# Kernel optimization log

Measured on AMD Instinct MI355X. Metric: run time of the kernel, lower is better.

The kernel has to match this reference:

```python
import jax, jax.numpy as jnp
import numpy as np

B, T, N, D = 64, 10, 64, 4      # batch, time steps, num_vars, input_size
H = 128                          # encoder_hidden
K = 2                            # num_edge_types
EPS = 1e-5                       # BatchNorm eps
_edges = np.ones((N, N)) - np.eye(N)
SEND = jnp.asarray(np.where(_edges)[0])   # [E], E = N*(N-1)
RECV = jnp.asarray(np.where(_edges)[1])   # [E]


def _xavier(key, shape):
    std = (2.0 / (shape[0] + shape[1])) ** 0.5
    return std * jax.random.normal(key, shape, dtype=jnp.float32)


def _mlp(x, w1, b1, w2, b2, g, beta):
    # RefNRIMLP: Linear -> ELU -> (dropout p=0) -> Linear -> ELU -> BatchNorm1d
    h = jax.nn.elu(x @ w1 + b1)
    h = jax.nn.elu(h @ w2 + b2)
    flat = h.reshape(-1, h.shape[-1])  # BN over flattened (batch*objects) axis
    mu = flat.mean(0)
    var = flat.var(0)
    flat = (flat - mu) * jax.lax.rsqrt(var + EPS) * g + beta
    return flat.reshape(h.shape)


def setup_inputs() -> dict:
    key = jax.random.key(0)
    ks = jax.random.split(key, 10)
    inp = {"inputs": jax.random.normal(ks[0], (B, T, N, D), dtype=jnp.float32)}
    fan_ins = {"mlp1": T * D, "mlp2": 2 * H, "mlp3": H, "mlp4": 3 * H}
    for i, (name, nin) in enumerate(fan_ins.items()):
        k1, k2 = jax.random.split(ks[i + 1])
        inp[name + "_w1"] = _xavier(k1, (nin, H))
        inp[name + "_b1"] = jnp.full((H,), 0.1, dtype=jnp.float32)
        inp[name + "_w2"] = _xavier(k2, (H, H))
        inp[name + "_b2"] = jnp.full((H,), 0.1, dtype=jnp.float32)
        inp[name + "_g"] = jnp.ones((H,), dtype=jnp.float32)
        inp[name + "_beta"] = jnp.zeros((H,), dtype=jnp.float32)
    inp["fc_w"] = _xavier(ks[9], (H, K))
    inp["fc_b"] = jnp.full((K,), 0.1, dtype=jnp.float32)
    return inp


def reference(inputs, mlp1_w1, mlp1_b1, mlp1_w2, mlp1_b2, mlp1_g, mlp1_beta,
              mlp2_w1, mlp2_b1, mlp2_w2, mlp2_b2, mlp2_g, mlp2_beta,
              mlp3_w1, mlp3_b1, mlp3_w2, mlp3_b2, mlp3_g, mlp3_beta,
              mlp4_w1, mlp4_b1, mlp4_w2, mlp4_b2, mlp4_g, mlp4_beta,
              fc_w, fc_b):
    # [B,T,N,D] -> [B,N,T*D]
    x = jnp.transpose(inputs, (0, 2, 1, 3)).reshape(B, N, T * D)
    x = _mlp(x, mlp1_w1, mlp1_b1, mlp1_w2, mlp1_b2, mlp1_g, mlp1_beta)
    # node2edge: gather send/recv node embeddings, concat -> [B,E,2H]
    x = jnp.concatenate([x[:, SEND], x[:, RECV]], axis=-1)
    x = _mlp(x, mlp2_w1, mlp2_b1, mlp2_w2, mlp2_b2, mlp2_g, mlp2_beta)
    x_skip = x
    # edge2node: one-hot(recv).T matmul == segment_sum over recv index, then /(N-1)
    agg = jax.ops.segment_sum(jnp.swapaxes(x, 0, 1), RECV, num_segments=N)  # [N,B,H]
    x = jnp.swapaxes(agg, 0, 1) / (N - 1)  # [B,N,H]
    x = _mlp(x, mlp3_w1, mlp3_b1, mlp3_w2, mlp3_b2, mlp3_g, mlp3_beta)
    x = jnp.concatenate([x[:, SEND], x[:, RECV]], axis=-1)  # [B,E,2H]
    x = jnp.concatenate([x, x_skip], axis=-1)  # [B,E,3H]
    x = _mlp(x, mlp4_w1, mlp4_b1, mlp4_w2, mlp4_b2, mlp4_g, mlp4_beta)
    return x @ fc_w + fc_b  # logits [B, E, K]
```

## Files before the change

### kernel.cpp

```cpp
#include <hip/hip_runtime.h>

#define BN_EPS 1e-5f

using h8 = __attribute__((ext_vector_type(8))) _Float16;
using f4v = __attribute__((ext_vector_type(4))) float;

#define OFF_COEF 0
#define OFF_CVEC 1024
#define OFF_H1 4096
#define OFF_P2 528384
#define OFF_Q2 1052672
#define OFF_H3 1576960
#define OFF_P4 2101248
#define OFF_Q4 2625536
#define OFF_W2P 3149824
#define OFF_W4P 3158016
#define OFF_WCP 3166208
#define OFF_H4B 3174400
#define WS_BYTES 78757888ull

__device__ __forceinline__ float elu_f(float x) {
    return x > 0.f ? x : __expf(x) - 1.f;
}

__device__ __forceinline__ unsigned short bf16r(float x) {
    unsigned u = __float_as_uint(x);
    return (unsigned short)((u + 0x7fffu + ((u >> 16) & 1u)) >> 16);
}


__device__ __forceinline__ void gemm_acc(float acc[4][8], float a0, float a1, float a2,
                                         float a3, const float4 wa, const float4 wb) {
    const float w[8] = {wa.x, wa.y, wa.z, wa.w, wb.x, wb.y, wb.z, wb.w};
    const float a[4] = {a0, a1, a2, a3};
#pragma unroll
    for (int j = 0; j < 4; ++j)
#pragma unroll
        for (int u = 0; u < 8; ++u)
            acc[j][u] = fmaf(a[j], w[u], acc[j][u]);
}

__device__ __forceinline__ void gemm_globalW(const float* As, int lda,
                                             const float* __restrict__ Wg, int K,
                                             float acc[4][8], int tx, int ty) {
    const float4* Wg4 = (const float4*)Wg;
#pragma unroll 4
    for (int k = 0; k < K; ++k) {
        float a0 = As[ty * lda + k];
        float a1 = As[(ty + 16) * lda + k];
        float a2 = As[(ty + 32) * lda + k];
        float a3 = As[(ty + 48) * lda + k];
        float4 wa = Wg4[k * 32 + tx];
        float4 wb = Wg4[k * 32 + 16 + tx];
        gemm_acc(acc, a0, a1, a2, a3, wa, wb);
    }
}

__device__ __forceinline__ void bias_elu(const float acc[4][8], const float* __restrict__ bias,
                                         float vals[4][8], int tx) {
    int ca = 4 * tx, cb = 64 + 4 * tx;
    float bv[8] = {bias[ca], bias[ca + 1], bias[ca + 2], bias[ca + 3],
                   bias[cb], bias[cb + 1], bias[cb + 2], bias[cb + 3]};
#pragma unroll
    for (int j = 0; j < 4; ++j)
#pragma unroll
        for (int u = 0; u < 8; ++u)
            vals[j][u] = elu_f(acc[j][u] + bv[u]);
}

__device__ __forceinline__ void store_tile(float* __restrict__ out, int row0,
                                           const float vals[4][8], int tx, int ty) {
#pragma unroll
    for (int j = 0; j < 4; ++j) {
        int r = row0 + ty + 16 * j;
        *(float4*)(out + r * 128 + 4 * tx) =
            make_float4(vals[j][0], vals[j][1], vals[j][2], vals[j][3]);
        *(float4*)(out + r * 128 + 64 + 4 * tx) =
            make_float4(vals[j][4], vals[j][5], vals[j][6], vals[j][7]);
    }
}

__device__ __forceinline__ void stats_tail(const float vals[4][8], float* red,
                                           float* __restrict__ st, int tid, int tx, int ty) {
    float ls[8], lq[8];
#pragma unroll
    for (int u = 0; u < 8; ++u) {
        ls[u] = vals[0][u] + vals[1][u] + vals[2][u] + vals[3][u];
        lq[u] = vals[0][u] * vals[0][u] + vals[1][u] * vals[1][u] +
                vals[2][u] * vals[2][u] + vals[3][u] * vals[3][u];
    }
    __syncthreads();
    int ca = 4 * tx, cb = 64 + 4 * tx;
#pragma unroll
    for (int u = 0; u < 4; ++u) {
        red[ty * 128 + ca + u] = ls[u];
        red[2048 + ty * 128 + ca + u] = lq[u];
        red[ty * 128 + cb + u] = ls[u + 4];
        red[2048 + ty * 128 + cb + u] = lq[u + 4];
    }
    __syncthreads();
    if (tid < 128) {
        float s = 0.f, q = 0.f;
#pragma unroll
        for (int t = 0; t < 16; ++t) {
            s += red[t * 128 + tid];
            q += red[2048 + t * 128 + tid];
        }
        atomicAdd(st + tid, s);
        atomicAdd(st + 128 + tid, q);
    }
}


__device__ __forceinline__ void gemm2_gw(const _Float16* A0, const _Float16* A1,
                                         const _Float16* __restrict__ wp,
                                         f4v acc0[4][2], f4v acc1[4][2], int lane, int w) {
#pragma unroll
    for (int kc = 0; kc < 4; ++kc) {
        h8 bf0 = *(const h8*)&wp[(((w * 2 + 0) * 4 + kc) * 64 + lane) * 8];
        h8 bf1 = *(const h8*)&wp[(((w * 2 + 1) * 4 + kc) * 64 + lane) * 8];
        h8 af0[4], af1[4];
#pragma unroll
        for (int rt = 0; rt < 4; ++rt) {
            af0[rt] = *(const h8*)&A0[((rt * 4 + kc) * 64 + lane) * 8];
            af1[rt] = *(const h8*)&A1[((rt * 4 + kc) * 64 + lane) * 8];
        }
#pragma unroll
        for (int rt = 0; rt < 4; ++rt) {
            acc0[rt][0] = __builtin_amdgcn_mfma_f32_16x16x32_f16(af0[rt], bf0, acc0[rt][0], 0, 0, 0);
            acc1[rt][0] = __builtin_amdgcn_mfma_f32_16x16x32_f16(af1[rt], bf0, acc1[rt][0], 0, 0, 0);
        }
#pragma unroll
        for (int rt = 0; rt < 4; ++rt) {
            acc0[rt][1] = __builtin_amdgcn_mfma_f32_16x16x32_f16(af0[rt], bf1, acc0[rt][1], 0, 0, 0);
            acc1[rt][1] = __builtin_amdgcn_mfma_f32_16x16x32_f16(af1[rt], bf1, acc1[rt][1], 0, 0, 0);
        }
    }
}

__device__ __forceinline__ void mfma_gemm_gw(const _Float16* Afr,
                                             const _Float16* __restrict__ wp,
                                             f4v acc[4][2], int lane, int w) {
#pragma unroll
    for (int kc = 0; kc < 4; ++kc) {
        h8 bf0 = *(const h8*)&wp[(((w * 2 + 0) * 4 + kc) * 64 + lane) * 8];
        h8 bf1 = *(const h8*)&wp[(((w * 2 + 1) * 4 + kc) * 64 + lane) * 8];
        h8 af[4];
#pragma unroll
        for (int rt = 0; rt < 4; ++rt)
            af[rt] = *(const h8*)&Afr[((rt * 4 + kc) * 64 + lane) * 8];
#pragma unroll
        for (int rt = 0; rt < 4; ++rt)
            acc[rt][0] = __builtin_amdgcn_mfma_f32_16x16x32_f16(af[rt], bf0, acc[rt][0], 0, 0, 0);
#pragma unroll
        for (int rt = 0; rt < 4; ++rt)
            acc[rt][1] = __builtin_amdgcn_mfma_f32_16x16x32_f16(af[rt], bf1, acc[rt][1], 0, 0, 0);
    }
}

__device__ __forceinline__ void vals_to_afrag(_Float16* Afr, const float vals[4][2][4],
                                              int lane, int w) {
    int cl = lane & 15, quad = lane >> 4;
#pragma unroll
    for (int ctl = 0; ctl < 2; ++ctl) {
        int col = (w * 2 + ctl) * 16 + cl;
        int kc = col >> 5, o = (col >> 3) & 3, j = col & 7;
#pragma unroll
        for (int rt = 0; rt < 4; ++rt)
#pragma unroll
            for (int i = 0; i < 4; ++i) {
                int m = quad * 4 + i;
                Afr[((rt * 4 + kc) * 64 + o * 16 + m) * 8 + j] = (_Float16)vals[rt][ctl][i];
            }
    }
}


__global__ void k_prep(float* W, const float* __restrict__ w2src,
                       const float* __restrict__ w4src) {
    int blk = blockIdx.x, tid = threadIdx.x;
    if (blk < 193) {
        int i = blk * 256 + tid;
        if (i < 16384) W[OFF_P2 + i] = 0.f;
        else if (i < 32768) W[OFF_P4 + i - 16384] = 0.f;
        else if (i < 49152) W[OFF_Q4 + i - 32768] = 0.f;
        else if (i < 49280) W[OFF_CVEC + i - 49152] = 0.f;
    } else {
        int second = blk >= 201;
        const float* src = second ? w4src : w2src;
        _Float16* wp = (_Float16*)(W + (second ? OFF_W4P : OFF_W2P));
        int flat = (blk - (second ? 201 : 193)) * 256 + tid;
        int g = flat >> 6, L = flat & 63;
        int ct = g >> 2, kc = g & 3;
        int nn = ct * 16 + (L & 15), k0 = kc * 32 + (L >> 4) * 8;
        h8 v;
#pragma unroll
        for (int j = 0; j < 8; ++j) v[j] = (_Float16)src[(k0 + j) * 128 + nn];
        *(h8*)&wp[flat * 8] = v;
    }
}

__global__ void k_finalize(const float* __restrict__ sums, float* __restrict__ coef,
                           float invM, const float* __restrict__ g,
                           const float* __restrict__ beta, float* __restrict__ zbuf) {
    int c = threadIdx.x;
    float s = 0.f, q = 0.f;
#pragma unroll 8
    for (int t = 0; t < 64; ++t) {
        s += sums[t * 256 + c];
        q += sums[t * 256 + 128 + c];
    }
    float mean = s * invM;
    float var = q * invM - mean * mean;
    float a = g[c] * rsqrtf(var + BN_EPS);
    coef[c] = a;
    coef[128 + c] = beta[c] - mean * a;
    if (zbuf)
        for (int i = c; i < 16384; i += 128) zbuf[i] = 0.f;
}

__global__ __launch_bounds__(256) void k_mlp1(const float* __restrict__ x,
                                              const float* __restrict__ w1,
                                              const float* __restrict__ b1,
                                              const float* __restrict__ w2,
                                              const float* __restrict__ b2,
                                              float* __restrict__ h1, float* __restrict__ st) {
    __shared__ float Xs[64 * 44];
    __shared__ float As[64 * 132];
    int tid = threadIdx.x, tx = tid & 15, ty = tid >> 4;
    int r0 = blockIdx.x * 64;
    for (int idx = tid; idx < 64 * 40; idx += 256) {
        int r = idx / 40, k = idx - r * 40;
        int rr = r0 + r, b = rr >> 6, n = rr & 63, t = k >> 2, d = k & 3;
        Xs[r * 44 + k] = x[((b * 10 + t) * 64 + n) * 4 + d];
    }
    __syncthreads();
    float acc[4][8] = {};
    gemm_globalW(Xs, 44, w1, 40, acc, tx, ty);
    float vals[4][8];
    bias_elu(acc, b1, vals, tx);
    int ca = 4 * tx, cb = 64 + 4 * tx;
#pragma unroll
    for (int j = 0; j < 4; ++j) {
        int r = ty + 16 * j;
#pragma unroll
        for (int u = 0; u < 4; ++u) {
            As[r * 132 + ca + u] = vals[j][u];
            As[r * 132 + cb + u] = vals[j][u + 4];
        }
    }
    __syncthreads();
    float acc2[4][8] = {};
    gemm_globalW(As, 132, w2, 128, acc2, tx, ty);
    float vals2[4][8];
    bias_elu(acc2, b2, vals2, tx);
    store_tile(h1, r0, vals2, tx, ty);
    stats_tail(vals2, As, st + (blockIdx.x & 63) * 256, tid, tx, ty);
}

__global__ __launch_bounds__(256) void k_pq(const float* __restrict__ h,
                                            const float* __restrict__ coef,
                                            const float* __restrict__ w,
                                            float* __restrict__ P, float* __restrict__ Q) {
    __shared__ float As[64 * 132];
    int tid = threadIdx.x, tx = tid & 15, ty = tid >> 4;
    int half = blockIdx.x >> 6;
    int r0 = (blockIdx.x & 63) * 64;
    const float* Wg = w + half * 128 * 128;
    float* out = half ? Q : P;
    const float4* h4 = (const float4*)h;
    const float4* av = (const float4*)coef;
    const float4* cv = (const float4*)(coef + 128);
#pragma unroll
    for (int i = 0; i < 8; ++i) {
        int f4 = tid + i * 256;
        int r = f4 >> 5, c4 = f4 & 31;
        float4 hv = h4[(r0 + r) * 32 + c4];
        float4 a = av[c4], c = cv[c4];
        float4 v;
        v.x = a.x * hv.x + c.x;
        v.y = a.y * hv.y + c.y;
        v.z = a.z * hv.z + c.z;
        v.w = a.w * hv.w + c.w;
        *(float4*)(As + r * 132 + c4 * 4) = v;
    }
    __syncthreads();
    float acc[4][8] = {};
    gemm_globalW(As, 132, Wg, 128, acc, tx, ty);
#pragma unroll
    for (int j = 0; j < 4; ++j) {
        int r = r0 + ty + 16 * j;
        *(float4*)(out + r * 128 + 4 * tx) = make_float4(acc[j][0], acc[j][1], acc[j][2], acc[j][3]);
        *(float4*)(out + r * 128 + 64 + 4 * tx) = make_float4(acc[j][4], acc[j][5], acc[j][6], acc[j][7]);
    }
}

__global__ __launch_bounds__(256, 4) void k_mlp2agg(const float* __restrict__ P2,
                                                    const float* __restrict__ Q2,
                                                    const float* __restrict__ b1,
                                                    const _Float16* __restrict__ w2p,
                                                    const float* __restrict__ b2,
                                                    float* __restrict__ aggraw,
                                                    _Float16* __restrict__ h2,
                                                    float* __restrict__ st) {
    __shared__ _Float16 Afr[8192];
    int tid = threadIdx.x;
    int lane = tid & 63, w = tid >> 6;
    int b = blockIdx.x >> 6, n = blockIdx.x & 63;
    float* stc = st + (blockIdx.x & 63) * 256;
    {
        int r = lane, kc = w;
        int s = (r < 63) ? (r + (r >= n ? 1 : 0)) : n;
        const float4* Pr = (const float4*)(P2 + (b * 64 + s) * 128);
        const float4* Qr = (const float4*)(Q2 + (b * 64 + n) * 128);
        const float4* B1 = (const float4*)b1;
        int rt = r >> 4, m = r & 15;
#pragma unroll
        for (int o = 0; o < 4; ++o) {
            int c4 = kc * 8 + o * 2;
            float4 p0 = Pr[c4], q0 = Qr[c4], bb0 = B1[c4];
            float4 p1 = Pr[c4 + 1], q1 = Qr[c4 + 1], bb1 = B1[c4 + 1];
            h8 v;
            v[0] = (_Float16)elu_f(p0.x + q0.x + bb0.x);
            v[1] = (_Float16)elu_f(p0.y + q0.y + bb0.y);
            v[2] = (_Float16)elu_f(p0.z + q0.z + bb0.z);
            v[3] = (_Float16)elu_f(p0.w + q0.w + bb0.w);
            v[4] = (_Float16)elu_f(p1.x + q1.x + bb1.x);
            v[5] = (_Float16)elu_f(p1.y + q1.y + bb1.y);
            v[6] = (_Float16)elu_f(p1.z + q1.z + bb1.z);
            v[7] = (_Float16)elu_f(p1.w + q1.w + bb1.w);
            *(h8*)&Afr[((rt * 4 + kc) * 64 + o * 16 + m) * 8] = v;
        }
    }
    __syncthreads();
    f4v acc[4][2];
#pragma unroll
    for (int rt = 0; rt < 4; ++rt)
#pragma unroll
        for (int c = 0; c < 2; ++c) acc[rt][c] = (f4v){0.f, 0.f, 0.f, 0.f};
    mfma_gemm_gw(Afr, w2p, acc, lane, w);
    int cl = lane & 15, quad = lane >> 4;
    float vals[2][4][4];
#pragma unroll
    for (int ctl = 0; ctl < 2; ++ctl) {
        int col = (w * 2 + ctl) * 16 + cl;
        float bias = b2[col];
        float s1 = 0.f, s2 = 0.f;
#pragma unroll
        for (int rt = 0; rt < 4; ++rt)
#pragma unroll
            for (int i = 0; i < 4; ++i) {
                int row = rt * 16 + quad * 4 + i;
                float v = elu_f(acc[rt][ctl][i] + bias);
                if (row == 63) v = 0.f;
                vals[ctl][rt][i] = v;
                s1 += v;
                s2 += v * v;
            }
        s1 += __shfl_xor(s1, 16);
        s2 += __shfl_xor(s2, 16);
        s1 += __shfl_xor(s1, 32);
        s2 += __shfl_xor(s2, 32);
        if (quad == 0) {
            aggraw[(b * 64 + n) * 128 + col] = s1;
            atomicAdd(stc + col, s1);
            atomicAdd(stc + 128 + col, s2);
        }
    }
    __syncthreads();
    unsigned short* Tb = (unsigned short*)Afr;
#pragma unroll
    for (int ctl = 0; ctl < 2; ++ctl) {
        int col = (w * 2 + ctl) * 16 + cl;
#pragma unroll
        for (int rt = 0; rt < 4; ++rt)
#pragma unroll
            for (int i = 0; i < 4; ++i) {
                int row = rt * 16 + quad * 4 + i;
                _Float16 hv = (_Float16)vals[ctl][rt][i];
                Tb[row * 128 + col] = *(unsigned short*)&hv;
            }
    }
    __syncthreads();
    {
        int rr = tid >> 2, cq = tid & 3;
        if (rr < 63) {
            int s = rr + (rr >= n ? 1 : 0);
            int e = s * 63 + (s > n ? n : n - 1);
            unsigned short* dst = (unsigned short*)h2 + ((size_t)b * 4032 + e) * 128;
#pragma unroll
            for (int i = 0; i < 4; ++i) {
                int off = cq * 32 + i * 8;
                *(uint4*)(dst + off) = *(uint4*)&Tb[rr * 128 + off];
            }
        }
    }
}

__global__ void k_wcprep(const float* __restrict__ w41, const float* __restrict__ coef2,
                         _Float16* __restrict__ wcp, float* __restrict__ cvec) {
    int k = blockIdx.x, c = threadIdx.x;
    float wv = w41[(256 + k) * 128 + c];
    int g = (c >> 4) * 4 + (k >> 5);
    int L = ((k >> 3) & 3) * 16 + (c & 15);
    int j = k & 7;
    wcp[(g * 64 + L) * 8 + j] = (_Float16)(coef2[k] * wv);
    atomicAdd(&cvec[c], coef2[128 + k] * wv);
}

__global__ __launch_bounds__(256) void k_mlp3(const float* __restrict__ raw,
                                              const float* __restrict__ coef2,
                                              const float* __restrict__ w1,
                                              const float* __restrict__ b1,
                                              const float* __restrict__ w2,
                                              const float* __restrict__ b2,
                                              float* __restrict__ h3, float* __restrict__ st) {
    __shared__ float As[64 * 132];
    int tid = threadIdx.x, tx = tid & 15, ty = tid >> 4;
    int r0 = blockIdx.x * 64;
    const float4* in4 = (const float4*)raw;
    const float4* av = (const float4*)coef2;
    const float4* cv = (const float4*)(coef2 + 128);
    const float inv63 = 1.f / 63.f;
#pragma unroll
    for (int i = 0; i < 8; ++i) {
        int f4 = tid + i * 256;
        int r = f4 >> 5, c4 = f4 & 31;
        float4 hv = in4[(r0 + r) * 32 + c4];
        float4 a = av[c4], c = cv[c4];
        float4 v;
        v.x = a.x * hv.x * inv63 + c.x;
        v.y = a.y * hv.y * inv63 + c.y;
        v.z = a.z * hv.z * inv63 + c.z;
        v.w = a.w * hv.w * inv63 + c.w;
        *(float4*)(As + r * 132 + c4 * 4) = v;
    }
    __syncthreads();
    float acc[4][8] = {};
    gemm_globalW(As, 132, w1, 128, acc, tx, ty);
    float vals[4][8];
    bias_elu(acc, b1, vals, tx);
    __syncthreads();
    int ca = 4 * tx, cb = 64 + 4 * tx;
#pragma unroll
    for (int j = 0; j < 4; ++j) {
        int r = ty + 16 * j;
#pragma unroll
        for (int u = 0; u < 4; ++u) {
            As[r * 132 + ca + u] = vals[j][u];
            As[r * 132 + cb + u] = vals[j][u + 4];
        }
    }
    __syncthreads();
    float acc2[4][8] = {};
    gemm_globalW(As, 132, w2, 128, acc2, tx, ty);
    float vals2[4][8];
    bias_elu(acc2, b2, vals2, tx);
    store_tile(h3, r0, vals2, tx, ty);
    stats_tail(vals2, As, st + (blockIdx.x & 63) * 256, tid, tx, ty);
}

__global__ __launch_bounds__(256, 3) void k_mlp4r2(const _Float16* __restrict__ h2,
                                                   const float* __restrict__ P4,
                                                   const float* __restrict__ Q4,
                                                   const _Float16* __restrict__ wcp,
                                                   const float* __restrict__ cvec,
                                                   const float* __restrict__ b1,
                                                   const _Float16* __restrict__ w4p2,
                                                   const float* __restrict__ b2,
                                                   unsigned short* __restrict__ h4,
                                                   float* __restrict__ st) {
    __shared__ _Float16 Afr0[8192];
    __shared__ _Float16 Afr1[8192];
    int tid = threadIdx.x;
    int lane = tid & 63, w = tid >> 6, cl = lane & 15, quad = lane >> 4;
    unsigned t0 = 2u * blockIdx.x, t1 = t0 + 1u;
    unsigned b0 = t0 / 63, b1i = t1 / 63;
    unsigned e00 = (t0 - b0 * 63) * 64, e01 = (t1 - b1i * 63) * 64;
    int row00 = t0 * 64, row01 = t1 * 64;
    float* stc = st + (blockIdx.x & 63) * 256;
#pragma unroll
    for (int i = 0; i < 4; ++i) {
        int u = tid + i * 256;
        int r = u >> 4, cu = u & 15;
        int dst = (((r >> 4) * 4 + (cu >> 2)) * 64 + (cu & 3) * 16 + (r & 15)) * 8;
        *(h8*)&Afr0[dst] = *(const h8*)&h2[(size_t)(row00 + r) * 128 + cu * 8];
        *(h8*)&Afr1[dst] = *(const h8*)&h2[(size_t)(row01 + r) * 128 + cu * 8];
    }
    __syncthreads();
    f4v acc0[4][2], acc1[4][2];
#pragma unroll
    for (int rt = 0; rt < 4; ++rt)
#pragma unroll
        for (int c = 0; c < 2; ++c) {
            acc0[rt][c] = (f4v){0.f, 0.f, 0.f, 0.f};
            acc1[rt][c] = (f4v){0.f, 0.f, 0.f, 0.f};
        }
    gemm2_gw(Afr0, Afr1, wcp, acc0, acc1, lane, w);
    float v0[4][2][4], v1[4][2][4];
    {
        int col0 = w * 32 + cl, col1 = col0 + 16;
        float base0 = b1[col0] + cvec[col0];
        float base1 = b1[col1] + cvec[col1];
#pragma unroll
        for (int rt = 0; rt < 4; ++rt)
#pragma unroll
            for (int i = 0; i < 4; ++i) {
                int rr = rt * 16 + quad * 4 + i;
                {
                    unsigned e = e00 + rr;
                    unsigned s = e / 63;
                    unsigned jj = e - s * 63;
                    unsigned rv = jj + (jj >= s ? 1u : 0u);
                    const float* Pr = P4 + (b0 * 64 + s) * 128;
                    const float* Qr = Q4 + (b0 * 64 + rv) * 128;
                    v0[rt][0][i] = elu_f(acc0[rt][0][i] + Pr[col0] + Qr[col0] + base0);
                    v0[rt][1][i] = elu_f(acc0[rt][1][i] + Pr[col1] + Qr[col1] + base1);
                }
                {
                    unsigned e = e01 + rr;
                    unsigned s = e / 63;
                    unsigned jj = e - s * 63;
                    unsigned rv = jj + (jj >= s ? 1u : 0u);
                    const float* Pr = P4 + (b1i * 64 + s) * 128;
                    const float* Qr = Q4 + (b1i * 64 + rv) * 128;
                    v1[rt][0][i] = elu_f(acc1[rt][0][i] + Pr[col0] + Qr[col0] + base0);
                    v1[rt][1][i] = elu_f(acc1[rt][1][i] + Pr[col1] + Qr[col1] + base1);
                }
            }
    }
    __syncthreads();
    vals_to_afrag(Afr0, v0, lane, w);
    vals_to_afrag(Afr1, v1, lane, w);
    __syncthreads();
#pragma unroll
    for (int rt = 0; rt < 4; ++rt)
#pragma unroll
        for (int c = 0; c < 2; ++c) {
            acc0[rt][c] = (f4v){0.f, 0.f, 0.f, 0.f};
            acc1[rt][c] = (f4v){0.f, 0.f, 0.f, 0.f};
        }
    gemm2_gw(Afr0, Afr1, w4p2, acc0, acc1, lane, w);
#pragma unroll
    for (int ctl = 0; ctl < 2; ++ctl) {
        int col = (w * 2 + ctl) * 16 + cl;
        float bias = b2[col];
        float s1 = 0.f, s2 = 0.f;
#pragma unroll
        for (int rt = 0; rt < 4; ++rt)
#pragma unroll
            for (int i = 0; i < 4; ++i) {
                float va = elu_f(acc0[rt][ctl][i] + bias);
                float vb = elu_f(acc1[rt][ctl][i] + bias);
                v0[rt][ctl][i] = va;
                v1[rt][ctl][i] = vb;
                s1 += va + vb;
                s2 += va * va + vb * vb;
            }
        s1 += __shfl_xor(s1, 16);
        s2 += __shfl_xor(s2, 16);
        s1 += __shfl_xor(s1, 32);
        s2 += __shfl_xor(s2, 32);
        if (quad == 0) {
            atomicAdd(stc + col, s1);
            atomicAdd(stc + 128 + col, s2);
        }
    }
    __syncthreads();
    unsigned short* T0 = (unsigned short*)Afr0;
    unsigned short* T1 = (unsigned short*)Afr1;
#pragma unroll
    for (int ctl = 0; ctl < 2; ++ctl) {
        int col = (w * 2 + ctl) * 16 + cl;
#pragma unroll
        for (int rt = 0; rt < 4; ++rt)
#pragma unroll
            for (int i = 0; i < 4; ++i) {
                int rr = rt * 16 + quad * 4 + i;
                T0[rr * 128 + col] = bf16r(v0[rt][ctl][i]);
                T1[rr * 128 + col] = bf16r(v1[rt][ctl][i]);
            }
    }
    __syncthreads();
    {
        int rr = tid >> 2, cq = tid & 3;
#pragma unroll
        for (int i = 0; i < 4; ++i) {
            int off = rr * 128 + cq * 32 + i * 8;
            *(uint4*)(h4 + (size_t)row00 * 128 + off) = *(uint4*)&T0[off];
            *(uint4*)(h4 + (size_t)row01 * 128 + off) = *(uint4*)&T1[off];
        }
    }
}

__global__ __launch_bounds__(256) void k_out(const unsigned short* __restrict__ h4,
                                             const float* __restrict__ coef4,
                                             const float* __restrict__ fcw,
                                             const float* __restrict__ fcb,
                                             float* __restrict__ out) {
    int tid = threadIdx.x;
    int lane = tid & 31, rsub = tid >> 5;
    int row = blockIdx.x * 8 + rsub;
    uint2 u = ((const uint2*)(h4 + (size_t)row * 128))[lane];
    float x0 = __uint_as_float(u.x << 16);
    float x1 = __uint_as_float(u.x & 0xffff0000u);
    float x2 = __uint_as_float(u.y << 16);
    float x3 = __uint_as_float(u.y & 0xffff0000u);
    float4 a = ((const float4*)coef4)[lane];
    float4 c = ((const float4*)(coef4 + 128))[lane];
    x0 = a.x * x0 + c.x;
    x1 = a.y * x1 + c.y;
    x2 = a.z * x2 + c.z;
    x3 = a.w * x3 + c.w;
    const float4* W = (const float4*)(fcw + lane * 8);
    float4 w01 = W[0], w23 = W[1];
    float s0 = x0 * w01.x + x1 * w01.z + x2 * w23.x + x3 * w23.z;
    float s1 = x0 * w01.y + x1 * w01.w + x2 * w23.y + x3 * w23.w;
#pragma unroll
    for (int off = 16; off > 0; off >>= 1) {
        s0 += __shfl_down(s0, off, 32);
        s1 += __shfl_down(s1, off, 32);
    }
    if (lane == 0) {
        out[row * 2] = s0 + fcb[0];
        out[row * 2 + 1] = s1 + fcb[1];
    }
}


extern "C" void kernel_launch(void* const* d_in, const int* in_sizes, int n_in,
                              void* d_out, int out_size, void* d_ws, size_t ws_size,
                              hipStream_t stream) {
    const float* x = (const float*)d_in[0];
    const float* m1_w1 = (const float*)d_in[1];
    const float* m1_b1 = (const float*)d_in[2];
    const float* m1_w2 = (const float*)d_in[3];
    const float* m1_b2 = (const float*)d_in[4];
    const float* m1_g = (const float*)d_in[5];
    const float* m1_be = (const float*)d_in[6];
    const float* m2_w1 = (const float*)d_in[7];
    const float* m2_b1 = (const float*)d_in[8];
    const float* m2_w2 = (const float*)d_in[9];
    const float* m2_b2 = (const float*)d_in[10];
    const float* m2_g = (const float*)d_in[11];
    const float* m2_be = (const float*)d_in[12];
    const float* m3_w1 = (const float*)d_in[13];
    const float* m3_b1 = (const float*)d_in[14];
    const float* m3_w2 = (const float*)d_in[15];
    const float* m3_b2 = (const float*)d_in[16];
    const float* m3_g = (const float*)d_in[17];
    const float* m3_be = (const float*)d_in[18];
    const float* m4_w1 = (const float*)d_in[19];
    const float* m4_b1 = (const float*)d_in[20];
    const float* m4_w2 = (const float*)d_in[21];
    const float* m4_b2 = (const float*)d_in[22];
    const float* m4_g = (const float*)d_in[23];
    const float* m4_be = (const float*)d_in[24];
    const float* fc_w = (const float*)d_in[25];
    const float* fc_b = (const float*)d_in[26];
    float* out = (float*)d_out;

    float* W = (float*)d_ws;
    float* coef1 = W + OFF_COEF;
    float* coef2 = W + OFF_COEF + 256;
    float* coef3 = W + OFF_COEF + 512;
    float* coef4 = W + OFF_COEF + 768;
    float* cvec = W + OFF_CVEC;
    float* h1 = W + OFF_H1;
    float* aggraw = h1;
    float* sums4 = h1;
    float* P2 = W + OFF_P2;
    float* sums1 = P2;
    float* Q2 = W + OFF_Q2;
    float* h3 = W + OFF_H3;
    float* P4 = W + OFF_P4;
    float* sums2 = P4;
    float* Q4 = W + OFF_Q4;
    float* sums3 = Q4;
    _Float16* w2p2 = (_Float16*)(W + OFF_W2P);
    _Float16* w4p2 = (_Float16*)(W + OFF_W4P);
    _Float16* wcp = (_Float16*)(W + OFF_WCP);
    _Float16* h2f = (_Float16*)(W + OFF_H4B);
    unsigned short* h4b = (unsigned short*)(W + OFF_H4B);

    if (ws_size < WS_BYTES) return;

    k_prep<<<209, 256, 0, stream>>>(W, m2_w2, m4_w2);
    k_mlp1<<<64, 256, 0, stream>>>(x, m1_w1, m1_b1, m1_w2, m1_b2, h1, sums1);
    k_finalize<<<1, 128, 0, stream>>>(sums1, coef1, 1.f / 4096.f, m1_g, m1_be, nullptr);
    k_pq<<<128, 256, 0, stream>>>(h1, coef1, m2_w1, P2, Q2);
    k_mlp2agg<<<4096, 256, 0, stream>>>(P2, Q2, m2_b1, w2p2, m2_b2, aggraw, h2f, sums2);
    k_finalize<<<1, 128, 0, stream>>>(sums2, coef2, 1.f / 258048.f, m2_g, m2_be, nullptr);
    k_wcprep<<<128, 128, 0, stream>>>(m4_w1, coef2, wcp, cvec);
    k_mlp3<<<64, 256, 0, stream>>>(aggraw, coef2, m3_w1, m3_b1, m3_w2, m3_b2, h3, sums3);
    k_finalize<<<1, 128, 0, stream>>>(sums3, coef3, 1.f / 4096.f, m3_g, m3_be, sums4);
    k_pq<<<128, 256, 0, stream>>>(h3, coef3, m4_w1, P4, Q4);
    k_mlp4r2<<<2016, 256, 0, stream>>>(h2f, P4, Q4, wcp, cvec, m4_b1, w4p2, m4_b2,
                                       h4b, sums4);
    k_finalize<<<1, 128, 0, stream>>>(sums4, coef4, 1.f / 258048.f, m4_g, m4_be, nullptr);
    k_out<<<32256, 256, 0, stream>>>(h4b, coef4, fc_w, fc_b, out);
}
```

Before: 349.0 us.

## Process two receiver nodes per block, halve k_pq tiles, simplify index math

k_mlp2agg now handles two receiver nodes per block with two shared A-fragment buffers and the shared gemm2_gw helper, so each loaded W2 fragment feeds twice as many MFMAs and there are half as many blocks and atomics. Its occupancy hint drops from 4 to 3 to fit the doubled shared memory and accumulators. k_pq uses 32-row tiles and twice as many blocks to fill more CUs. In k_mlp4r2 the per-element division by 63 and repeated P4 loads are replaced by precomputed sender rows and a select. h4 is stored as fp16 instead of bf16, and k_out converts fp16 directly.

```diff
diff --git a/kernel.cpp b/kernel.cpp
--- a/kernel.cpp
+++ b/kernel.cpp
@@ -3,6 +3,7 @@
 #define BN_EPS 1e-5f
 
 using h8 = __attribute__((ext_vector_type(8))) _Float16;
+using h4v = __attribute__((ext_vector_type(4))) _Float16;
 using f4v = __attribute__((ext_vector_type(4))) float;
 
 #define OFF_COEF 0
@@ -23,11 +24,6 @@
     return x > 0.f ? x : __expf(x) - 1.f;
 }
 
-__device__ __forceinline__ unsigned short bf16r(float x) {
-    unsigned u = __float_as_uint(x);
-    return (unsigned short)((u + 0x7fffu + ((u >> 16) & 1u)) >> 16);
-}
-
 
 __device__ __forceinline__ void gemm_acc(float acc[4][8], float a0, float a1, float a2,
                                          float a3, const float4 wa, const float4 wb) {
@@ -138,26 +134,6 @@
     }
 }
 
-__device__ __forceinline__ void mfma_gemm_gw(const _Float16* Afr,
-                                             const _Float16* __restrict__ wp,
-                                             f4v acc[4][2], int lane, int w) {
-#pragma unroll
-    for (int kc = 0; kc < 4; ++kc) {
-        h8 bf0 = *(const h8*)&wp[(((w * 2 + 0) * 4 + kc) * 64 + lane) * 8];
-        h8 bf1 = *(const h8*)&wp[(((w * 2 + 1) * 4 + kc) * 64 + lane) * 8];
-        h8 af[4];
-#pragma unroll
-        for (int rt = 0; rt < 4; ++rt)
-            af[rt] = *(const h8*)&Afr[((rt * 4 + kc) * 64 + lane) * 8];
-#pragma unroll
-        for (int rt = 0; rt < 4; ++rt)
-            acc[rt][0] = __builtin_amdgcn_mfma_f32_16x16x32_f16(af[rt], bf0, acc[rt][0], 0, 0, 0);
-#pragma unroll
-        for (int rt = 0; rt < 4; ++rt)
-            acc[rt][1] = __builtin_amdgcn_mfma_f32_16x16x32_f16(af[rt], bf1, acc[rt][1], 0, 0, 0);
-    }
-}
-
 __device__ __forceinline__ void vals_to_afrag(_Float16* Afr, const float vals[4][2][4],
                                               int lane, int w) {
     int cl = lane & 15, quad = lane >> 4;
@@ -172,6 +148,28 @@
                 int m = quad * 4 + i;
                 Afr[((rt * 4 + kc) * 64 + o * 16 + m) * 8 + j] = (_Float16)vals[rt][ctl][i];
             }
+    }
+}
+
+__device__ __forceinline__ void stage_pair(_Float16* Afr, const float4* __restrict__ Pr,
+                                           const float4* __restrict__ Qr,
+                                           const float4* __restrict__ B1, int lane, int kc) {
+    int rt = lane >> 4, m = lane & 15;
+#pragma unroll
+    for (int o = 0; o < 4; ++o) {
+        int c4 = kc * 8 + o * 2;
+        float4 p0 = Pr[c4], q0 = Qr[c4], bb0 = B1[c4];
+        float4 p1 = Pr[c4 + 1], q1 = Qr[c4 + 1], bb1 = B1[c4 + 1];
+        h8 v;
+        v[0] = (_Float16)elu_f(p0.x + q0.x + bb0.x);
+        v[1] = (_Float16)elu_f(p0.y + q0.y + bb0.y);
+        v[2] = (_Float16)elu_f(p0.z + q0.z + bb0.z);
+        v[3] = (_Float16)elu_f(p0.w + q0.w + bb0.w);
+        v[4] = (_Float16)elu_f(p1.x + q1.x + bb1.x);
+        v[5] = (_Float16)elu_f(p1.y + q1.y + bb1.y);
+        v[6] = (_Float16)elu_f(p1.z + q1.z + bb1.z);
+        v[7] = (_Float16)elu_f(p1.w + q1.w + bb1.w);
+        *(h8*)&Afr[((rt * 4 + kc) * 64 + o * 16 + m) * 8] = v;
     }
 }
 
@@ -262,17 +260,17 @@
                                             const float* __restrict__ coef,
                                             const float* __restrict__ w,
                                             float* __restrict__ P, float* __restrict__ Q) {
-    __shared__ float As[64 * 132];
+    __shared__ float As[32 * 132];
     int tid = threadIdx.x, tx = tid & 15, ty = tid >> 4;
-    int half = blockIdx.x >> 6;
-    int r0 = (blockIdx.x & 63) * 64;
+    int half = blockIdx.x >> 7;
+    int r0 = (blockIdx.x & 127) * 32;
     const float* Wg = w + half * 128 * 128;
     float* out = half ? Q : P;
     const float4* h4 = (const float4*)h;
     const float4* av = (const float4*)coef;
     const float4* cv = (const float4*)(coef + 128);
 #pragma unroll
-    for (int i = 0; i < 8; ++i) {
+    for (int i = 0; i < 4; ++i) {
         int f4 = tid + i * 256;
         int r = f4 >> 5, c4 = f4 & 31;
         float4 hv = h4[(r0 + r) * 32 + c4];
@@ -285,17 +283,30 @@
         *(float4*)(As + r * 132 + c4 * 4) = v;
     }
     __syncthreads();
-    float acc[4][8] = {};
-    gemm_globalW(As, 132, Wg, 128, acc, tx, ty);
-#pragma unroll
-    for (int j = 0; j < 4; ++j) {
+    float acc[2][8] = {};
+    const float4* Wg4 = (const float4*)Wg;
+#pragma unroll 4
+    for (int k = 0; k < 128; ++k) {
+        float a0 = As[ty * 132 + k];
+        float a1 = As[(ty + 16) * 132 + k];
+        float4 wa = Wg4[k * 32 + tx];
+        float4 wb = Wg4[k * 32 + 16 + tx];
+        const float wv[8] = {wa.x, wa.y, wa.z, wa.w, wb.x, wb.y, wb.z, wb.w};
+#pragma unroll
+        for (int u = 0; u < 8; ++u) {
+            acc[0][u] = fmaf(a0, wv[u], acc[0][u]);
+            acc[1][u] = fmaf(a1, wv[u], acc[1][u]);
+        }
+    }
+#pragma unroll
+    for (int j = 0; j < 2; ++j) {
         int r = r0 + ty + 16 * j;
         *(float4*)(out + r * 128 + 4 * tx) = make_float4(acc[j][0], acc[j][1], acc[j][2], acc[j][3]);
         *(float4*)(out + r * 128 + 64 + 4 * tx) = make_float4(acc[j][4], acc[j][5], acc[j][6], acc[j][7]);
     }
 }
 
-__global__ __launch_bounds__(256, 4) void k_mlp2agg(const float* __restrict__ P2,
+__global__ __launch_bounds__(256, 3) void k_mlp2agg(const float* __restrict__ P2,
                                                     const float* __restrict__ Q2,
                                                     const float* __restrict__ b1,
                                                     const _Float16* __restrict__ w2p,
@@ -303,72 +314,69 @@
                                                     float* __restrict__ aggraw,
                                                     _Float16* __restrict__ h2,
                                                     float* __restrict__ st) {
-    __shared__ _Float16 Afr[8192];
+    __shared__ _Float16 Afr0[8192];
+    __shared__ _Float16 Afr1[8192];
     int tid = threadIdx.x;
-    int lane = tid & 63, w = tid >> 6;
-    int b = blockIdx.x >> 6, n = blockIdx.x & 63;
+    int lane = tid & 63, w = tid >> 6, cl = lane & 15, quad = lane >> 4;
+    int b = blockIdx.x >> 5, j2 = blockIdx.x & 31;
+    int n0 = 2 * j2, n1 = n0 + 1;
     float* stc = st + (blockIdx.x & 63) * 256;
     {
-        int r = lane, kc = w;
-        int s = (r < 63) ? (r + (r >= n ? 1 : 0)) : n;
-        const float4* Pr = (const float4*)(P2 + (b * 64 + s) * 128);
-        const float4* Qr = (const float4*)(Q2 + (b * 64 + n) * 128);
+        int r = lane;
+        int s0 = (r < 63) ? (r + (r >= n0 ? 1 : 0)) : n0;
+        int s1i = (r < 63) ? (r + (r >= n1 ? 1 : 0)) : n1;
         const float4* B1 = (const float4*)b1;
-        int rt = r >> 4, m = r & 15;
-#pragma unroll
-        for (int o = 0; o < 4; ++o) {
-            int c4 = kc * 8 + o * 2;
-            float4 p0 = Pr[c4], q0 = Qr[c4], bb0 = B1[c4];
-            float4 p1 = Pr[c4 + 1], q1 = Qr[c4 + 1], bb1 = B1[c4 + 1];
-            h8 v;
-            v[0] = (_Float16)elu_f(p0.x + q0.x + bb0.x);
-            v[1] = (_Float16)elu_f(p0.y + q0.y + bb0.y);
-            v[2] = (_Float16)elu_f(p0.z + q0.z + bb0.z);
-            v[3] = (_Float16)elu_f(p0.w + q0.w + bb0.w);
-            v[4] = (_Float16)elu_f(p1.x + q1.x + bb1.x);
-            v[5] = (_Float16)elu_f(p1.y + q1.y + bb1.y);
-            v[6] = (_Float16)elu_f(p1.z + q1.z + bb1.z);
-            v[7] = (_Float16)elu_f(p1.w + q1.w + bb1.w);
-            *(h8*)&Afr[((rt * 4 + kc) * 64 + o * 16 + m) * 8] = v;
-        }
-    }
-    __syncthreads();
-    f4v acc[4][2];
+        stage_pair(Afr0, (const float4*)(P2 + (b * 64 + s0) * 128),
+                   (const float4*)(Q2 + (b * 64 + n0) * 128), B1, lane, w);
+        stage_pair(Afr1, (const float4*)(P2 + (b * 64 + s1i) * 128),
+                   (const float4*)(Q2 + (b * 64 + n1) * 128), B1, lane, w);
+    }
+    __syncthreads();
+    f4v acc0[4][2], acc1[4][2];
 #pragma unroll
     for (int rt = 0; rt < 4; ++rt)
 #pragma unroll
-        for (int c = 0; c < 2; ++c) acc[rt][c] = (f4v){0.f, 0.f, 0.f, 0.f};
-    mfma_gemm_gw(Afr, w2p, acc, lane, w);
-    int cl = lane & 15, quad = lane >> 4;
-    float vals[2][4][4];
+        for (int c = 0; c < 2; ++c) {
+            acc0[rt][c] = (f4v){0.f, 0.f, 0.f, 0.f};
+            acc1[rt][c] = (f4v){0.f, 0.f, 0.f, 0.f};
+        }
+    gemm2_gw(Afr0, Afr1, w2p, acc0, acc1, lane, w);
+    float v0[2][4][4], v1[2][4][4];
 #pragma unroll
     for (int ctl = 0; ctl < 2; ++ctl) {
         int col = (w * 2 + ctl) * 16 + cl;
         float bias = b2[col];
-        float s1 = 0.f, s2 = 0.f;
+        float a0 = 0.f, a1 = 0.f, sq = 0.f;
 #pragma unroll
         for (int rt = 0; rt < 4; ++rt)
 #pragma unroll
             for (int i = 0; i < 4; ++i) {
                 int row = rt * 16 + quad * 4 + i;
-                float v = elu_f(acc[rt][ctl][i] + bias);
-                if (row == 63) v = 0.f;
-                vals[ctl][rt][i] = v;
-                s1 += v;
-                s2 += v * v;
+                float va = elu_f(acc0[rt][ctl][i] + bias);
+                float vb = elu_f(acc1[rt][ctl][i] + bias);
+                if (row == 63) { va = 0.f; vb = 0.f; }
+                v0[ctl][rt][i] = va;
+                v1[ctl][rt][i] = vb;
+                a0 += va;
+                a1 += vb;
+                sq += va * va + vb * vb;
             }
-        s1 += __shfl_xor(s1, 16);
-        s2 += __shfl_xor(s2, 16);
-        s1 += __shfl_xor(s1, 32);
-        s2 += __shfl_xor(s2, 32);
+        a0 += __shfl_xor(a0, 16);
+        a1 += __shfl_xor(a1, 16);
+        sq += __shfl_xor(sq, 16);
+        a0 += __shfl_xor(a0, 32);
+        a1 += __shfl_xor(a1, 32);
+        sq += __shfl_xor(sq, 32);
         if (quad == 0) {
-            aggraw[(b * 64 + n) * 128 + col] = s1;
-            atomicAdd(stc + col, s1);
-            atomicAdd(stc + 128 + col, s2);
-        }
-    }
-    __syncthreads();
-    unsigned short* Tb = (unsigned short*)Afr;
+            aggraw[(b * 64 + n0) * 128 + col] = a0;
+            aggraw[(b * 64 + n1) * 128 + col] = a1;
+            atomicAdd(stc + col, a0 + a1);
+            atomicAdd(stc + 128 + col, sq);
+        }
+    }
+    __syncthreads();
+    unsigned short* T0 = (unsigned short*)Afr0;
+    unsigned short* T1 = (unsigned short*)Afr1;
 #pragma unroll
     for (int ctl = 0; ctl < 2; ++ctl) {
         int col = (w * 2 + ctl) * 16 + cl;
@@ -377,21 +385,27 @@
 #pragma unroll
             for (int i = 0; i < 4; ++i) {
                 int row = rt * 16 + quad * 4 + i;
-                _Float16 hv = (_Float16)vals[ctl][rt][i];
-                Tb[row * 128 + col] = *(unsigned short*)&hv;
+                _Float16 ha = (_Float16)v0[ctl][rt][i];
+                _Float16 hb = (_Float16)v1[ctl][rt][i];
+                T0[row * 128 + col] = *(unsigned short*)&ha;
+                T1[row * 128 + col] = *(unsigned short*)&hb;
             }
     }
     __syncthreads();
     {
         int rr = tid >> 2, cq = tid & 3;
         if (rr < 63) {
-            int s = rr + (rr >= n ? 1 : 0);
-            int e = s * 63 + (s > n ? n : n - 1);
-            unsigned short* dst = (unsigned short*)h2 + ((size_t)b * 4032 + e) * 128;
+            int s0 = rr + (rr >= n0 ? 1 : 0);
+            int e0 = s0 * 63 + (s0 > n0 ? n0 : n0 - 1);
+            int s1i = rr + (rr >= n1 ? 1 : 0);
+            int e1 = s1i * 63 + (s1i > n1 ? n1 : n1 - 1);
+            unsigned short* d0 = (unsigned short*)h2 + ((size_t)b * 4032 + e0) * 128;
+            unsigned short* d1 = (unsigned short*)h2 + ((size_t)b * 4032 + e1) * 128;
 #pragma unroll
             for (int i = 0; i < 4; ++i) {
                 int off = cq * 32 + i * 8;
-                *(uint4*)(dst + off) = *(uint4*)&Tb[rr * 128 + off];
+                *(uint4*)(d0 + off) = *(uint4*)&T0[rr * 128 + off];
+                *(uint4*)(d1 + off) = *(uint4*)&T1[rr * 128 + off];
             }
         }
     }
@@ -502,6 +516,21 @@
         int col0 = w * 32 + cl, col1 = col0 + 16;
         float base0 = b1[col0] + cvec[col0];
         float base1 = b1[col1] + cvec[col1];
+        unsigned sA0 = e00 / 63, sA1 = e01 / 63;
+        unsigned baseE0 = sA0 * 63, baseE1 = sA1 * 63;
+        unsigned eB0 = baseE0 + 63, eB1 = baseE1 + 63;
+        unsigned sB0 = sA0 < 63u ? sA0 + 1u : sA0;
+        unsigned sB1 = sA1 < 63u ? sA1 + 1u : sA1;
+        const float* PA0 = P4 + (b0 * 64 + sA0) * 128;
+        const float* PB0 = P4 + (b0 * 64 + sB0) * 128;
+        const float* PA1 = P4 + (b1i * 64 + sA1) * 128;
+        const float* PB1 = P4 + (b1i * 64 + sB1) * 128;
+        float pA0c0 = PA0[col0], pA0c1 = PA0[col1];
+        float pB0c0 = PB0[col0], pB0c1 = PB0[col1];
+        float pA1c0 = PA1[col0], pA1c1 = PA1[col1];
+        float pB1c0 = PB1[col0], pB1c1 = PB1[col1];
+        const float* Qb0 = Q4 + (size_t)b0 * 64 * 128;
+        const float* Qb1 = Q4 + (size_t)b1i * 64 * 128;
 #pragma unroll
         for (int rt = 0; rt < 4; ++rt)
 #pragma unroll
@@ -509,23 +538,25 @@
                 int rr = rt * 16 + quad * 4 + i;
                 {
                     unsigned e = e00 + rr;
-                    unsigned s = e / 63;
-                    unsigned jj = e - s * 63;
+                    bool hi = e >= eB0;
+                    unsigned s = hi ? sB0 : sA0;
+                    unsigned jj = e - (hi ? eB0 : baseE0);
                     unsigned rv = jj + (jj >= s ? 1u : 0u);
-                    const float* Pr = P4 + (b0 * 64 + s) * 128;
-                    const float* Qr = Q4 + (b0 * 64 + rv) * 128;
-                    v0[rt][0][i] = elu_f(acc0[rt][0][i] + Pr[col0] + Qr[col0] + base0);
-                    v0[rt][1][i] = elu_f(acc0[rt][1][i] + Pr[col1] + Qr[col1] + base1);
+                    const float* Qr = Qb0 + rv * 128;
+                    float p0 = hi ? pB0c0 : pA0c0, p1 = hi ? pB0c1 : pA0c1;
+                    v0[rt][0][i] = elu_f(acc0[rt][0][i] + p0 + Qr[col0] + base0);
+                    v0[rt][1][i] = elu_f(acc0[rt][1][i] + p1 + Qr[col1] + base1);
                 }
                 {
                     unsigned e = e01 + rr;
-                    unsigned s = e / 63;
-                    unsigned jj = e - s * 63;
+                    bool hi = e >= eB1;
+                    unsigned s = hi ? sB1 : sA1;
+                    unsigned jj = e - (hi ? eB1 : baseE1);
                     unsigned rv = jj + (jj >= s ? 1u : 0u);
-                    const float* Pr = P4 + (b1i * 64 + s) * 128;
-                    const float* Qr = Q4 + (b1i * 64 + rv) * 128;
-                    v1[rt][0][i] = elu_f(acc1[rt][0][i] + Pr[col0] + Qr[col0] + base0);
-                    v1[rt][1][i] = elu_f(acc1[rt][1][i] + Pr[col1] + Qr[col1] + base1);
+                    const float* Qr = Qb1 + rv * 128;
+                    float p0 = hi ? pB1c0 : pA1c0, p1 = hi ? pB1c1 : pA1c1;
+                    v1[rt][0][i] = elu_f(acc1[rt][0][i] + p0 + Qr[col0] + base0);
+                    v1[rt][1][i] = elu_f(acc1[rt][1][i] + p1 + Qr[col1] + base1);
                 }
             }
     }
@@ -577,8 +608,10 @@
 #pragma unroll
             for (int i = 0; i < 4; ++i) {
                 int rr = rt * 16 + quad * 4 + i;
-                T0[rr * 128 + col] = bf16r(v0[rt][ctl][i]);
-                T1[rr * 128 + col] = bf16r(v1[rt][ctl][i]);
+                _Float16 ha = (_Float16)v0[rt][ctl][i];
+                _Float16 hb = (_Float16)v1[rt][ctl][i];
+                T0[rr * 128 + col] = *(unsigned short*)&ha;
+                T1[rr * 128 + col] = *(unsigned short*)&hb;
             }
     }
     __syncthreads();
@@ -601,11 +634,8 @@
     int tid = threadIdx.x;
     int lane = tid & 31, rsub = tid >> 5;
     int row = blockIdx.x * 8 + rsub;
-    uint2 u = ((const uint2*)(h4 + (size_t)row * 128))[lane];
-    float x0 = __uint_as_float(u.x << 16);
-    float x1 = __uint_as_float(u.x & 0xffff0000u);
-    float x2 = __uint_as_float(u.y << 16);
-    float x3 = __uint_as_float(u.y & 0xffff0000u);
+    h4v hv = ((const h4v*)(h4 + (size_t)row * 128))[lane];
+    float x0 = (float)hv[0], x1 = (float)hv[1], x2 = (float)hv[2], x3 = (float)hv[3];
     float4 a = ((const float4*)coef4)[lane];
     float4 c = ((const float4*)(coef4 + 128))[lane];
     x0 = a.x * x0 + c.x;
@@ -688,13 +718,13 @@
     k_prep<<<209, 256, 0, stream>>>(W, m2_w2, m4_w2);
     k_mlp1<<<64, 256, 0, stream>>>(x, m1_w1, m1_b1, m1_w2, m1_b2, h1, sums1);
     k_finalize<<<1, 128, 0, stream>>>(sums1, coef1, 1.f / 4096.f, m1_g, m1_be, nullptr);
-    k_pq<<<128, 256, 0, stream>>>(h1, coef1, m2_w1, P2, Q2);
-    k_mlp2agg<<<4096, 256, 0, stream>>>(P2, Q2, m2_b1, w2p2, m2_b2, aggraw, h2f, sums2);
+    k_pq<<<256, 256, 0, stream>>>(h1, coef1, m2_w1, P2, Q2);
+    k_mlp2agg<<<2048, 256, 0, stream>>>(P2, Q2, m2_b1, w2p2, m2_b2, aggraw, h2f, sums2);
     k_finalize<<<1, 128, 0, stream>>>(sums2, coef2, 1.f / 258048.f, m2_g, m2_be, nullptr);
     k_wcprep<<<128, 128, 0, stream>>>(m4_w1, coef2, wcp, cvec);
     k_mlp3<<<64, 256, 0, stream>>>(aggraw, coef2, m3_w1, m3_b1, m3_w2, m3_b2, h3, sums3);
     k_finalize<<<1, 128, 0, stream>>>(sums3, coef3, 1.f / 4096.f, m3_g, m3_be, sums4);
-    k_pq<<<128, 256, 0, stream>>>(h3, coef3, m4_w1, P4, Q4);
+    k_pq<<<256, 256, 0, stream>>>(h3, coef3, m4_w1, P4, Q4);
     k_mlp4r2<<<2016, 256, 0, stream>>>(h2f, P4, Q4, wcp, cvec, m4_b1, w4p2, m4_b2,
                                        h4b, sums4);
     k_finalize<<<1, 128, 0, stream>>>(sums4, coef4, 1.f / 258048.f, m4_g, m4_be, nullptr);
```

After: 347.2 us. No clear change (-0.5%).
